# Kernel optimization log

Measured on AMD Instinct MI355X. Metric: run time of the kernel, lower is better.

The kernel has to match this reference:

```python
import jax, jax.numpy as jnp
import numpy as np

FF = 2          # freqfold
HALF_FF = 1     # ff // 2

def _fold_k(t, G, ff):
    # t: [N, G, D] -> real/imag each [N, nband, G*ff]
    N, _, D = t.shape
    Df = D // 2
    nband = Df // ff
    t = jnp.swapaxes(t, -1, -2)  # [N, D, G]
    def fold(x):  # x: [N, Df, G]
        x = x.reshape(N, nband, ff, G).transpose(0, 2, 1, 3)  # [N, ff, nband, G]
        return x.reshape(N, nband, G * ff)
    return fold(t[:, :Df, :]), fold(t[:, Df:, :])

def _fold_q(t, G, groups, ff):
    # t: [N, H, D] with H = G*groups -> real/imag each [N, groups, nband, G*ff]
    N, H, D = t.shape
    Df = D // 2
    nband = Df // ff
    t = t.reshape(N, G, groups, D).transpose(0, 2, 1, 3)  # [N, groups, G, D]
    t = jnp.swapaxes(t, -1, -2)                            # [N, groups, D, G]
    def fold(x):  # x: [N, groups, Df, G]
        x = x.reshape(N, groups, nband, ff, G).transpose(0, 1, 3, 2, 4)  # [N, groups, ff, nband, G]
        return x.reshape(N, groups, nband, G * ff)
    return fold(t[:, :, :Df, :]), fold(t[:, :, Df:, :])

def setup_inputs() -> dict:
    key = jax.random.key(0)
    ks = jax.random.split(key, 8)
    N, H, G, D, r = 8192, 32, 8, 128, 4
    ff = FF
    nband = D // (2 * ff)
    gff = G * ff
    nope_in = G * D - D // 2
    return {
        "q": jax.random.normal(ks[0], (N, H, D), jnp.float32),
        "k": jax.random.normal(ks[1], (N, G, D), jnp.float32),
        "v": jax.random.normal(ks[2], (N, G, D), jnp.float32),
        "q_orig": jax.random.normal(ks[3], (N, H, D), jnp.float32),
        "k_orig": jax.random.normal(ks[4], (N, G, D), jnp.float32),
        "qk_index_proj": 0.02 * jax.random.normal(ks[5], (nband, gff, gff), jnp.float32),
        "qk_nope_proj_w": 0.02 * jax.random.normal(ks[6], (D // 2, nope_in), jnp.float32),
        "v_transform": 0.02 * jax.random.normal(ks[7], (H, D, r), jnp.float32),
    }

def reference(q, k, v, q_orig, k_orig, qk_index_proj, qk_nope_proj_w, v_transform):
    N, H, D = q.shape
    G = k.shape[1]
    groups = H // G
    ff, half_ff = FF, HALF_FF
    nband = D // (2 * ff)
    nope_cols = G * ff - half_ff
    qk_w = qk_index_proj

    # ---- rope path (post-RoPE q, k) ----
    kr_re, kr_im = _fold_k(k, G, ff)
    kr_re_p = jnp.einsum('bnf,nfr->bnr', kr_re, qk_w)
    kr_im_p = jnp.einsum('bnf,nfr->bnr', kr_im, qk_w)
    index_k_rope = jnp.concatenate([
        kr_re_p[:, :, :half_ff].reshape(N, nband * half_ff),
        kr_im_p[:, :, :half_ff].reshape(N, nband * half_ff)], axis=-1)

    qr_re, qr_im = _fold_q(q, G, groups, ff)
    qr_re_p = jnp.einsum('tgnf,nfr->tgnr', qr_re, qk_w)
    qr_im_p = jnp.einsum('tgnf,nfr->tgnr', qr_im, qk_w)
    index_q_rope = jnp.concatenate([
        qr_re_p[:, :, :, :half_ff].reshape(N, groups, nband * half_ff),
        qr_im_p[:, :, :, :half_ff].reshape(N, groups, nband * half_ff)], axis=-1)

    # ---- nope path (pre-RoPE q_orig, k_orig) ----
    kn_re, kn_im = _fold_k(k_orig, G, ff)
    kn_re_p = jnp.einsum('bnf,nfr->bnr', kn_re, qk_w)
    kn_im_p = jnp.einsum('bnf,nfr->bnr', kn_im, qk_w)
    k_nope_rotary = jnp.concatenate([
        kn_re_p[:, :, half_ff:].reshape(N, nband * nope_cols),
        kn_im_p[:, :, half_ff:].reshape(N, nband * nope_cols)], axis=-1)
    k_nope_lr = k_nope_rotary @ qk_nope_proj_w.T
    index_k = jnp.concatenate([index_k_rope, k_nope_lr], axis=-1)  # [N, D]

    qn_re, qn_im = _fold_q(q_orig, G, groups, ff)
    qn_re_p = jnp.einsum('tgnf,nfr->tgnr', qn_re, qk_w)
    qn_im_p = jnp.einsum('tgnf,nfr->tgnr', qn_im, qk_w)
    q_nope_rotary = jnp.concatenate([
        qn_re_p[:, :, :, half_ff:].reshape(N, groups, nband * nope_cols),
        qn_im_p[:, :, :, half_ff:].reshape(N, groups, nband * nope_cols)], axis=-1)
    q_nope_lr = q_nope_rotary @ qk_nope_proj_w.T
    index_q = jnp.concatenate([index_q_rope, q_nope_lr], axis=-1)  # [N, groups, D]

    # ---- per-head weights from V ----
    r = v_transform.shape[-1]
    v_h = jnp.repeat(v, groups, axis=1)  # [N, H, D]
    w = jnp.einsum('nhd,hdr->nhr', v_h, v_transform)
    w = w.reshape(N, G, groups, r).transpose(0, 2, 1, 3).reshape(N, groups, G * r)
    weights = jnp.linalg.norm(w.astype(jnp.float32), axis=-1)  # [N, groups]

    return index_q, index_k, weights
```

## Files before the change

kernel.cpp:

```cpp
#include <hip/hip_runtime.h>
#include <math.h>

namespace {
constexpr int N_TOK  = 8192;
constexpr int GROUPS = 4;
constexpr int D      = 128;
}

typedef short v8s __attribute__((ext_vector_type(8)));
typedef float v4f __attribute__((ext_vector_type(4)));

__device__ __forceinline__ short f2bf(float f) {
    union { float f; unsigned u; } x; x.f = f;
    unsigned r = x.u + 0x7FFFu + ((x.u >> 16) & 1u);
    return (short)(r >> 16);
}

__global__ __launch_bounds__(256)
void build_MT(const float* __restrict__ widx,
              const float* __restrict__ wn,
              short* __restrict__ MT)
{
    const int idx = blockIdx.x * 256 + threadIdx.x;
    const int col = idx >> 10;
    const int kk  = idx & 1023;
    const int g   = kk >> 7;
    const int dp  = kk & 127;
    const int part = dp >> 6;
    const int dpp  = dp & 63;
    const int B    = (dpp & 1) * 16 + (dpp >> 2);
    const int c    = g + 8 * ((dpp >> 1) & 1);

    float val;
    if (col < 64) {
        val = (col == part * 32 + B) ? widx[B * 256 + c * 16] : 0.f;
    } else {
        const int d2 = col - 64;
        const float* wrow = wn + d2 * 960 + part * 480 + B * 15;
        const float* wi   = widx + B * 256 + c * 16;
        float s = 0.f;
#pragma unroll
        for (int o = 1; o < 16; ++o) s += wi[o] * wrow[o - 1];
        val = s;
    }
    MT[idx] = f2bf(val);
}

__global__ __launch_bounds__(256)
void gemm_kernel(const float* __restrict__ q,
                 const float* __restrict__ k,
                 const float* __restrict__ q_orig,
                 const float* __restrict__ k_orig,
                 const short* __restrict__ MT,
                 float* __restrict__ out_iq,
                 float* __restrict__ out_ik)
{
    const int lane = threadIdx.x & 63;
    const int wave = threadIdx.x >> 6;
    const int m    = lane & 15;
    const int quad = lane >> 4;
    const int base_row = blockIdx.x * 64 + wave * 16;

    const int row = base_row + m;
    const int n   = row / 5;
    const int jj  = row - n * 5;
    const bool isq = (jj < 4);
    const float* ropep = isq ? (q      + n * 4096 + jj * 128) : (k      + n * 1024);
    const float* nopep = isq ? (q_orig + n * 4096 + jj * 128) : (k_orig + n * 1024);

    const short* bbase = MT + m * 1024;

    v4f acc[8];
#pragma unroll
    for (int t = 0; t < 8; ++t) acc[t] = (v4f){0.f, 0.f, 0.f, 0.f};

#pragma unroll 2
    for (int ks = 0; ks < 32; ++ks) {
        const int kk   = ks * 32 + quad * 8;
        const int offA = isq ? ((kk >> 7) * 512 + (kk & 127)) : kk;
        const float4 r0 = *(const float4*)(ropep + offA);
        const float4 r1 = *(const float4*)(ropep + offA + 4);
        const float4 n0 = *(const float4*)(nopep + offA);
        const float4 n1 = *(const float4*)(nopep + offA + 4);
        v8s ar, an;
        ar[0] = f2bf(r0.x); ar[1] = f2bf(r0.y); ar[2] = f2bf(r0.z); ar[3] = f2bf(r0.w);
        ar[4] = f2bf(r1.x); ar[5] = f2bf(r1.y); ar[6] = f2bf(r1.z); ar[7] = f2bf(r1.w);
        an[0] = f2bf(n0.x); an[1] = f2bf(n0.y); an[2] = f2bf(n0.z); an[3] = f2bf(n0.w);
        an[4] = f2bf(n1.x); an[5] = f2bf(n1.y); an[6] = f2bf(n1.z); an[7] = f2bf(n1.w);

        const short* bp = bbase + kk;
#pragma unroll
        for (int t = 0; t < 8; ++t) {
            const v8s b = *(const v8s*)(bp + t * 16384);
            acc[t] = __builtin_amdgcn_mfma_f32_16x16x32_bf16(
                         (t < 4) ? ar : an, b, acc[t], 0, 0, 0);
        }
    }

#pragma unroll
    for (int t = 0; t < 8; ++t) {
        const int col = t * 16 + m;
#pragma unroll
        for (int i = 0; i < 4; ++i) {
            const int r2  = base_row + quad * 4 + i;
            const int n2  = r2 / 5;
            const int jj2 = r2 - n2 * 5;
            float* dst = (jj2 < 4) ? (out_iq + n2 * 512 + jj2 * 128)
                                   : (out_ik + n2 * 128);
            dst[col] = acc[t][i];
        }
    }
}

__global__ __launch_bounds__(256)
void weights_kernel(const float* __restrict__ v,
                    const float* __restrict__ vt,
                    float* __restrict__ out_w)
{
    __shared__ float s_wsq[2][128];
    const int half = threadIdx.x >> 7;
    const int tid  = threadIdx.x & 127;
    const int tok  = blockIdx.x * 2 + half;
    const int h  = tid >> 2;
    const int rr = tid & 3;
    const int g  = h >> 2;
    const float* vrow = v  + tok * 1024 + g * 128;
    const float* vtp  = vt + h * 512 + rr;
    float acc = 0.f;
#pragma unroll 8
    for (int d = 0; d < 128; ++d) acc += vrow[d] * vtp[d * 4];
    s_wsq[half][tid] = acc * acc;
    __syncthreads();
    if (tid < 4) {
        float s = 0.f;
#pragma unroll
        for (int g2 = 0; g2 < 8; ++g2)
#pragma unroll
            for (int r2 = 0; r2 < 4; ++r2)
                s += s_wsq[half][(g2 * 4 + tid) * 4 + r2];
        out_w[tok * 4 + tid] = sqrtf(s);
    }
}

extern "C" void kernel_launch(void* const* d_in, const int* in_sizes, int n_in,
                              void* d_out, int out_size, void* d_ws, size_t ws_size,
                              hipStream_t stream) {
    const float* q      = (const float*)d_in[0];
    const float* k      = (const float*)d_in[1];
    const float* v      = (const float*)d_in[2];
    const float* q_orig = (const float*)d_in[3];
    const float* k_orig = (const float*)d_in[4];
    const float* widx   = (const float*)d_in[5];
    const float* wn     = (const float*)d_in[6];
    const float* vt     = (const float*)d_in[7];

    float* out_iq = (float*)d_out;
    float* out_ik = out_iq + (size_t)N_TOK * GROUPS * D;
    float* out_w  = out_ik + (size_t)N_TOK * D;

    short* MT = (short*)d_ws;

    hipLaunchKernelGGL(build_MT, dim3(512), dim3(256), 0, stream, widx, wn, MT);
    hipLaunchKernelGGL(gemm_kernel, dim3(640), dim3(256), 0, stream,
                       q, k, q_orig, k_orig, MT, out_iq, out_ik);
    hipLaunchKernelGGL(weights_kernel, dim3(4096), dim3(256), 0, stream,
                       v, vt, out_w);
}
```

Baseline: 474.1 us.

## Split rope path out of GEMM, shrink nope GEMM, restructure weights kernel

The rope half of the old combined GEMM was a mostly-zero matrix (one nonzero per column). It is replaced by a direct fp32 16-term dot product in a separate kernel, so the MFMA GEMM now covers only the 64 nope output columns. That GEMM stages bf16-converted A tiles in LDS through coalesced loads. The weights kernel now reads a pre-transposed v_transform table with float4 loads and reduces with wave shuffles instead of LDS. The cost is an extra kernel launch, and q and k are read by two separate kernels.

```diff
diff --git a/kernel.cpp b/kernel.cpp
--- a/kernel.cpp
+++ b/kernel.cpp
@@ -1,11 +1,5 @@
 #include <hip/hip_runtime.h>
 #include <math.h>
-
-namespace {
-constexpr int N_TOK  = 8192;
-constexpr int GROUPS = 4;
-constexpr int D      = 128;
-}
 
 typedef short v8s __attribute__((ext_vector_type(8)));
 typedef float v4f __attribute__((ext_vector_type(4)));
@@ -17,129 +11,175 @@
 }
 
 __global__ __launch_bounds__(256)
-void build_MT(const float* __restrict__ widx,
-              const float* __restrict__ wn,
-              short* __restrict__ MT)
+void build_tables(const float* __restrict__ widx,
+                  const float* __restrict__ wn,
+                  const float* __restrict__ vt,
+                  short* __restrict__ MnT,
+                  float* __restrict__ W2)
 {
     const int idx = blockIdx.x * 256 + threadIdx.x;
-    const int col = idx >> 10;
-    const int kk  = idx & 1023;
-    const int g   = kk >> 7;
-    const int dp  = kk & 127;
-    const int part = dp >> 6;
-    const int dpp  = dp & 63;
-    const int B    = (dpp & 1) * 16 + (dpp >> 2);
-    const int c    = g + 8 * ((dpp >> 1) & 1);
-
-    float val;
-    if (col < 64) {
-        val = (col == part * 32 + B) ? widx[B * 256 + c * 16] : 0.f;
-    } else {
-        const int d2 = col - 64;
-        const float* wrow = wn + d2 * 960 + part * 480 + B * 15;
+    if (idx < 65536) {
+        const int col = idx >> 10, kk = idx & 1023;
+        const int g = kk >> 7, dp = kk & 127;
+        const int part = dp >> 6, dpp = dp & 63;
+        const int B = (dpp & 1) * 16 + (dpp >> 2);
+        const int c = g + 8 * ((dpp >> 1) & 1);
+        const float* wrow = wn + col * 960 + part * 480 + B * 15;
         const float* wi   = widx + B * 256 + c * 16;
         float s = 0.f;
 #pragma unroll
         for (int o = 1; o < 16; ++o) s += wi[o] * wrow[o - 1];
-        val = s;
-    }
-    MT[idx] = f2bf(val);
+        MnT[idx] = f2bf(s);
+    } else {
+        const int t = idx - 65536;
+        const int cc = t & 3, l = (t >> 2) & 63, i = (t >> 8) & 31, s = t >> 13;
+        const int h = (l >> 2) + 16 * s, rr = l & 3, d = i * 4 + cc;
+        W2[t] = vt[h * 512 + d * 4 + rr];
+    }
+}
+
+constexpr int LDA = 264;
+
+__global__ __launch_bounds__(128)
+void nope_gemm(const float* __restrict__ q_orig,
+               const float* __restrict__ k_orig,
+               const short* __restrict__ MnT,
+               float* __restrict__ out_iq,
+               float* __restrict__ out_ik)
+{
+    __shared__ short sA[32 * LDA];
+    const int tid  = threadIdx.x;
+    const int lane = tid & 63, wave = tid >> 6;
+    const int m    = lane & 15, quad = lane >> 4;
+    const bool isQ = blockIdx.x < 1024;
+
+    v4f acc[4];
+#pragma unroll
+    for (int t = 0; t < 4; ++t) acc[t] = (v4f){0.f, 0.f, 0.f, 0.f};
+
+    for (int c = 0; c < 4; ++c) {
+        if (isQ) {
+            const float* src = q_orig + (size_t)blockIdx.x * 32768 + c * 1024;
+#pragma unroll
+            for (int i = 0; i < 16; ++i) {
+                const int e  = (i * 128 + tid) * 4;
+                const int np = e >> 10, r8 = e & 1023;
+                const float4 f = *(const float4*)(src + np * 4096 + r8);
+                const int hl = r8 >> 7, dp = r8 & 127;
+                const int row = np * 4 + (hl & 3);
+                const int lk  = (hl >> 2) * 128 + dp;
+                short4 b4 = { f2bf(f.x), f2bf(f.y), f2bf(f.z), f2bf(f.w) };
+                *(short4*)&sA[row * LDA + lk] = b4;
+            }
+        } else {
+            const float* src = k_orig + (size_t)(blockIdx.x - 1024) * 32768 + c * 256;
+#pragma unroll
+            for (int i = 0; i < 16; ++i) {
+                const int e  = (i * 128 + tid) * 4;
+                const int np = e >> 8, lk = e & 255;
+                const float4 f = *(const float4*)(src + np * 1024 + lk);
+                short4 b4 = { f2bf(f.x), f2bf(f.y), f2bf(f.z), f2bf(f.w) };
+                *(short4*)&sA[np * LDA + lk] = b4;
+            }
+        }
+        __syncthreads();
+        const short* arow = sA + (wave * 16 + m) * LDA;
+#pragma unroll
+        for (int ks = 0; ks < 8; ++ks) {
+            const v8s a = *(const v8s*)(arow + ks * 32 + quad * 8);
+            const int kglob = c * 256 + ks * 32 + quad * 8;
+#pragma unroll
+            for (int ct = 0; ct < 4; ++ct) {
+                const v8s b = *(const v8s*)(MnT + (ct * 16 + m) * 1024 + kglob);
+                acc[ct] = __builtin_amdgcn_mfma_f32_16x16x32_bf16(a, b, acc[ct], 0, 0, 0);
+            }
+        }
+        __syncthreads();
+    }
+
+#pragma unroll
+    for (int ct = 0; ct < 4; ++ct) {
+        const int col = 64 + ct * 16 + m;
+#pragma unroll
+        for (int i = 0; i < 4; ++i) {
+            const int row = wave * 16 + quad * 4 + i;
+            if (isQ) {
+                const int tok = blockIdx.x * 8 + (row >> 2);
+                out_iq[(size_t)tok * 512 + (row & 3) * 128 + col] = acc[ct][i];
+            } else {
+                const int tok = (blockIdx.x - 1024) * 32 + row;
+                out_ik[(size_t)tok * 128 + col] = acc[ct][i];
+            }
+        }
+    }
 }
 
 __global__ __launch_bounds__(256)
-void gemm_kernel(const float* __restrict__ q,
+void rope_kernel(const float* __restrict__ q,
                  const float* __restrict__ k,
-                 const float* __restrict__ q_orig,
-                 const float* __restrict__ k_orig,
-                 const short* __restrict__ MT,
+                 const float* __restrict__ widx,
                  float* __restrict__ out_iq,
                  float* __restrict__ out_ik)
 {
-    const int lane = threadIdx.x & 63;
-    const int wave = threadIdx.x >> 6;
-    const int m    = lane & 15;
-    const int quad = lane >> 4;
-    const int base_row = blockIdx.x * 64 + wave * 16;
-
-    const int row = base_row + m;
-    const int n   = row / 5;
-    const int jj  = row - n * 5;
-    const bool isq = (jj < 4);
-    const float* ropep = isq ? (q      + n * 4096 + jj * 128) : (k      + n * 1024);
-    const float* nopep = isq ? (q_orig + n * 4096 + jj * 128) : (k_orig + n * 1024);
-
-    const short* bbase = MT + m * 1024;
-
-    v4f acc[8];
-#pragma unroll
-    for (int t = 0; t < 8; ++t) acc[t] = (v4f){0.f, 0.f, 0.f, 0.f};
-
-#pragma unroll 2
-    for (int ks = 0; ks < 32; ++ks) {
-        const int kk   = ks * 32 + quad * 8;
-        const int offA = isq ? ((kk >> 7) * 512 + (kk & 127)) : kk;
-        const float4 r0 = *(const float4*)(ropep + offA);
-        const float4 r1 = *(const float4*)(ropep + offA + 4);
-        const float4 n0 = *(const float4*)(nopep + offA);
-        const float4 n1 = *(const float4*)(nopep + offA + 4);
-        v8s ar, an;
-        ar[0] = f2bf(r0.x); ar[1] = f2bf(r0.y); ar[2] = f2bf(r0.z); ar[3] = f2bf(r0.w);
-        ar[4] = f2bf(r1.x); ar[5] = f2bf(r1.y); ar[6] = f2bf(r1.z); ar[7] = f2bf(r1.w);
-        an[0] = f2bf(n0.x); an[1] = f2bf(n0.y); an[2] = f2bf(n0.z); an[3] = f2bf(n0.w);
-        an[4] = f2bf(n1.x); an[5] = f2bf(n1.y); an[6] = f2bf(n1.z); an[7] = f2bf(n1.w);
-
-        const short* bp = bbase + kk;
-#pragma unroll
-        for (int t = 0; t < 8; ++t) {
-            const v8s b = *(const v8s*)(bp + t * 16384);
-            acc[t] = __builtin_amdgcn_mfma_f32_16x16x32_bf16(
-                         (t < 4) ? ar : an, b, acc[t], 0, 0, 0);
-        }
-    }
-
-#pragma unroll
-    for (int t = 0; t < 8; ++t) {
-        const int col = t * 16 + m;
-#pragma unroll
-        for (int i = 0; i < 4; ++i) {
-            const int r2  = base_row + quad * 4 + i;
-            const int n2  = r2 / 5;
-            const int jj2 = r2 - n2 * 5;
-            float* dst = (jj2 < 4) ? (out_iq + n2 * 512 + jj2 * 128)
-                                   : (out_ik + n2 * 128);
-            dst[col] = acc[t][i];
-        }
+    const int lane = threadIdx.x & 63, wave = threadIdx.x >> 6;
+    const int col = lane, B = col & 31, part = col >> 5;
+
+    float wgt[16];
+#pragma unroll
+    for (int b = 0; b < 2; ++b)
+#pragma unroll
+        for (int g = 0; g < 8; ++g)
+            wgt[b * 8 + g] = widx[B * 256 + (g + 8 * b) * 16];
+
+    const int dp0 = part * 64 + 4 * (B & 15) + (B >> 4);
+    float acc = 0.f;
+    if (blockIdx.x < 8192) {
+        const float* src = q + (size_t)blockIdx.x * 4096 + wave * 128;
+#pragma unroll
+        for (int b = 0; b < 2; ++b)
+#pragma unroll
+            for (int g = 0; g < 8; ++g)
+                acc += src[g * 512 + dp0 + 2 * b] * wgt[b * 8 + g];
+        out_iq[(size_t)blockIdx.x * 512 + wave * 128 + col] = acc;
+    } else {
+        const int n = (blockIdx.x - 8192) * 4 + wave;
+        const float* src = k + (size_t)n * 1024;
+#pragma unroll
+        for (int b = 0; b < 2; ++b)
+#pragma unroll
+            for (int g = 0; g < 8; ++g)
+                acc += src[g * 128 + dp0 + 2 * b] * wgt[b * 8 + g];
+        out_ik[(size_t)n * 128 + col] = acc;
     }
 }
 
 __global__ __launch_bounds__(256)
 void weights_kernel(const float* __restrict__ v,
-                    const float* __restrict__ vt,
+                    const float* __restrict__ W2,
                     float* __restrict__ out_w)
 {
-    __shared__ float s_wsq[2][128];
-    const int half = threadIdx.x >> 7;
-    const int tid  = threadIdx.x & 127;
-    const int tok  = blockIdx.x * 2 + half;
-    const int h  = tid >> 2;
-    const int rr = tid & 3;
-    const int g  = h >> 2;
-    const float* vrow = v  + tok * 1024 + g * 128;
-    const float* vtp  = vt + h * 512 + rr;
-    float acc = 0.f;
+    const int lane = threadIdx.x & 63, wave = threadIdx.x >> 6;
+    const int n = blockIdx.x * 4 + wave;
+    const int g1 = lane >> 4;
+    const float4* v1 = (const float4*)(v + (size_t)n * 1024 + g1 * 128);
+    const float4* v2 = (const float4*)(v + (size_t)n * 1024 + (g1 + 4) * 128);
+    const float4* w1 = (const float4*)(W2) + lane;
+    const float4* w2 = (const float4*)(W2 + 8192) + lane;
+    float a1 = 0.f, a2 = 0.f;
 #pragma unroll 8
-    for (int d = 0; d < 128; ++d) acc += vrow[d] * vtp[d * 4];
-    s_wsq[half][tid] = acc * acc;
-    __syncthreads();
-    if (tid < 4) {
-        float s = 0.f;
-#pragma unroll
-        for (int g2 = 0; g2 < 8; ++g2)
-#pragma unroll
-            for (int r2 = 0; r2 < 4; ++r2)
-                s += s_wsq[half][(g2 * 4 + tid) * 4 + r2];
-        out_w[tok * 4 + tid] = sqrtf(s);
-    }
+    for (int i = 0; i < 32; ++i) {
+        const float4 x1 = v1[i], x2 = v2[i];
+        const float4 y1 = w1[i * 64], y2 = w2[i * 64];
+        a1 += x1.x * y1.x + x1.y * y1.y + x1.z * y1.z + x1.w * y1.w;
+        a2 += x2.x * y2.x + x2.y * y2.y + x2.z * y2.z + x2.w * y2.w;
+    }
+    float s = a1 * a1 + a2 * a2;
+    s += __shfl_xor(s, 1);
+    s += __shfl_xor(s, 2);
+    s += __shfl_xor(s, 16);
+    s += __shfl_xor(s, 32);
+    if ((lane & 51) == 0)
+        out_w[(size_t)n * 4 + (lane >> 2)] = sqrtf(s);
 }
 
 extern "C" void kernel_launch(void* const* d_in, const int* in_sizes, int n_in,
@@ -155,14 +195,18 @@
     const float* vt     = (const float*)d_in[7];
 
     float* out_iq = (float*)d_out;
-    float* out_ik = out_iq + (size_t)N_TOK * GROUPS * D;
-    float* out_w  = out_ik + (size_t)N_TOK * D;
-
-    short* MT = (short*)d_ws;
-
-    hipLaunchKernelGGL(build_MT, dim3(512), dim3(256), 0, stream, widx, wn, MT);
-    hipLaunchKernelGGL(gemm_kernel, dim3(640), dim3(256), 0, stream,
-                       q, k, q_orig, k_orig, MT, out_iq, out_ik);
-    hipLaunchKernelGGL(weights_kernel, dim3(4096), dim3(256), 0, stream,
-                       v, vt, out_w);
-}
+    float* out_ik = out_iq + (size_t)8192 * 512;
+    float* out_w  = out_ik + (size_t)8192 * 128;
+
+    short* MnT = (short*)d_ws;
+    float* W2  = (float*)((char*)d_ws + 131072);
+
+    hipLaunchKernelGGL(build_tables, dim3(320), dim3(256), 0, stream,
+                       widx, wn, vt, MnT, W2);
+    hipLaunchKernelGGL(nope_gemm, dim3(1280), dim3(128), 0, stream,
+                       q_orig, k_orig, MnT, out_iq, out_ik);
+    hipLaunchKernelGGL(rope_kernel, dim3(10240), dim3(256), 0, stream,
+                       q, k, widx, out_iq, out_ik);
+    hipLaunchKernelGGL(weights_kernel, dim3(2048), dim3(256), 0, stream,
+                       v, W2, out_w);
+}
```

Result: slower. 494.1 us (+4.2%).
